# Optimization experiments

Hardware: AMD Instinct MI355X
Metric: run time of the kernel (lower is better)

The kernel has to match this reference:

```python
import jax, jax.numpy as jnp
import numpy as np

B, D, H, E, K = 8192, 1024, 4096, 8, 2
LOSS_COEF = 0.01
EPS_COMBINE = float(np.finfo(np.float64).eps)  # np.finfo(float).eps used in combine


def setup_inputs() -> dict:
    key = jax.random.key(0)
    ks = jax.random.split(key, 6)
    s_in = 1.0 / np.sqrt(D)
    s_hid = 1.0 / np.sqrt(H)
    return {
        "x": jax.random.normal(ks[0], (B, D), jnp.float32),
        "w_gate": jax.random.uniform(ks[1], (E, D), jnp.float32, -s_in, s_in),
        "fc1_w": jax.random.uniform(ks[2], (E, H, D), jnp.float32, -s_in, s_in),
        "fc1_b": jax.random.uniform(ks[3], (E, H), jnp.float32, -s_in, s_in),
        "fc2_w": jax.random.uniform(ks[4], (E, D, H), jnp.float32, -s_hid, s_hid),
        "fc2_b": jax.random.uniform(ks[5], (E, D), jnp.float32, -s_hid, s_hid),
    }


def _cv_squared(v):
    # torch .var() uses ddof=1
    return jnp.var(v, ddof=1) / (jnp.mean(v) ** 2 + 1e-10)


def _top_k_gating(x, w_gate):
    # clean logits (noisy_gating=False): [B, E]
    logits = x @ w_gate.T
    top_vals, top_idx = jax.lax.top_k(logits, K + 1)  # min(k+1, E)
    topk_vals = top_vals[:, :K]
    topk_idx = top_idx[:, :K]
    topk_gates = jax.nn.softmax(topk_vals, axis=1)
    gates = jnp.zeros((x.shape[0], E), x.dtype)
    gates = gates.at[jnp.arange(x.shape[0])[:, None], topk_idx].set(topk_gates)
    return gates


def _forward(x, w_gate, fc1_w, fc1_b, fc2_w, fc2_b):
    gates = _top_k_gating(x, w_gate)            # [B, E], sparse (k nonzeros/row)
    importance = gates.sum(axis=0)              # [E]
    load = (gates > 0).sum(axis=0).astype(jnp.float32)
    loss = (_cv_squared(importance) + _cv_squared(load)) * LOSS_COEF

    # Dense-equivalent expert compute: tokens with gate==0 contribute 0 to the
    # combine, identical math to SparseDispatcher's gather/scatter.
    h = jnp.einsum('bd,ehd->beh', x, fc1_w) + fc1_b            # [B, E, H]
    h = jax.nn.gelu(h, approximate=False)                      # torch exact gelu
    o = jnp.einsum('beh,edh->bed', h, fc2_w) + fc2_b           # [B, E, D]
    log_p = jax.nn.log_softmax(o, axis=-1)                     # LogSoftmax(dim=1)

    # combine: exp, weight by gates, scatter-add, eps-fill, log
    combined = jnp.einsum('be,bed->bd', gates, jnp.exp(log_p)) # [B, D]
    combined = jnp.where(combined == 0, EPS_COMBINE, combined)
    y = jnp.log(combined)
    return y, loss


def reference(x, w_gate, fc1_w, fc1_b, fc2_w, fc2_b):
    return _forward(x, w_gate, fc1_w, fc1_b, fc2_w, fc2_b)
```

## Files before the change

kernel.cpp:

```cpp
#include <hip/hip_runtime.h>
#include <cstdint>
#include <cmath>

#define BT 8192
#define DD 1024
#define HH 4096
#define EE 8

typedef __attribute__((ext_vector_type(8))) short short8;
typedef __attribute__((ext_vector_type(4))) float f32x4;
typedef unsigned short u16;
typedef unsigned int u32;

__device__ __forceinline__ u16 f2bf(float f) {
    u32 u = __float_as_uint(f);
    u += 0x7FFFu + ((u >> 16) & 1u);
    return (u16)(u >> 16);
}

__device__ __forceinline__ void gld_lds16(const void* g, void* l) {
    __builtin_amdgcn_global_load_lds((__attribute__((address_space(1))) void*)g,
                                     (__attribute__((address_space(3))) void*)l,
                                     16, 0, 0);
}

__global__ void cvt_kernel(const float* __restrict__ src, u16* __restrict__ dst, int n8) {
    int i = blockIdx.x * blockDim.x + threadIdx.x;
    if (i >= n8) return;
    size_t base = (size_t)i * 8;
    float4 a = *(const float4*)(src + base);
    float4 b = *(const float4*)(src + base + 4);
    uint4 o;
    o.x = (u32)f2bf(a.x) | ((u32)f2bf(a.y) << 16);
    o.y = (u32)f2bf(a.z) | ((u32)f2bf(a.w) << 16);
    o.z = (u32)f2bf(b.x) | ((u32)f2bf(b.y) << 16);
    o.w = (u32)f2bf(b.z) | ((u32)f2bf(b.w) << 16);
    *(uint4*)(dst + base) = o;
}

__global__ void gating_kernel(const float* __restrict__ x, const float* __restrict__ wg,
                              float* __restrict__ gate_arr, int* __restrict__ list,
                              int* __restrict__ info,
                              int* __restrict__ counts, float* __restrict__ importance) {
    int wave = (blockIdx.x * blockDim.x + threadIdx.x) >> 6;
    int lane = threadIdx.x & 63;
    if (wave >= BT) return;
    const float* xr = x + (size_t)wave * DD;
    double acc[EE];
#pragma unroll
    for (int e = 0; e < EE; ++e) acc[e] = 0.0;
    for (int i = lane; i < DD; i += 64) {
        double xv = (double)xr[i];
#pragma unroll
        for (int e = 0; e < EE; ++e)
            acc[e] += xv * (double)wg[e * DD + i];
    }
#pragma unroll
    for (int e = 0; e < EE; ++e) {
        double v = acc[e];
        for (int off = 32; off; off >>= 1) v += __shfl_down(v, off, 64);
        acc[e] = v;
    }
    if (lane == 0) {
        int i0 = 0; double v0 = acc[0];
        for (int e = 1; e < EE; ++e) if (acc[e] > v0) { v0 = acc[e]; i0 = e; }
        int i1 = -1; double v1 = -1e300;
        for (int e = 0; e < EE; ++e) { if (e == i0) continue; if (acc[e] > v1) { v1 = acc[e]; i1 = e; } }
        double e1 = exp(v1 - v0);
        double s = 1.0 + e1;
        float g0 = (float)(1.0 / s);
        float g1 = (float)(e1 / s);
        gate_arr[2 * wave]     = g0;
        gate_arr[2 * wave + 1] = g1;
        atomicAdd(&importance[i0], g0);
        atomicAdd(&importance[i1], g1);
        int p0 = atomicAdd(&counts[i0], 1);
        list[i0 * BT + p0] = wave;
        int p1 = atomicAdd(&counts[i1], 1);
        list[i1 * BT + p1] = wave;
        info[2 * wave]     = (i0 << 16) | p0;
        info[2 * wave + 1] = (i1 << 16) | p1;
    }
}

__global__ void loss_kernel(const int* __restrict__ counts, const float* __restrict__ importance,
                            int* __restrict__ offs, float* __restrict__ out_loss) {
    if (threadIdx.x == 0 && blockIdx.x == 0) {
        double mi = 0, ml = 0;
        int off = 0;
        for (int e = 0; e < EE; e++) {
            offs[e] = off; off += counts[e];
            mi += (double)importance[e]; ml += (double)counts[e];
        }
        mi /= EE; ml /= EE;
        double vi = 0, vl = 0;
        for (int e = 0; e < EE; e++) {
            double di = (double)importance[e] - mi; vi += di * di;
            double dl = (double)counts[e] - ml;     vl += dl * dl;
        }
        vi /= (EE - 1); vl /= (EE - 1);
        double cv_i = vi / (mi * mi + 1e-10);
        double cv_l = vl / (ml * ml + 1e-10);
        *out_loss = (float)((cv_i + cv_l) * 0.01);
    }
}

__global__ void gather_x_kernel(const float* __restrict__ x, const int* __restrict__ list,
                                const int* __restrict__ counts, const int* __restrict__ offs,
                                u16* __restrict__ xg) {
    int r = blockIdx.x;
    int e = 0;
#pragma unroll
    for (int i = 1; i < EE; ++i) if (r >= offs[i]) e = i;
    int m = r - offs[e];
    if (m >= counts[e]) return;
    int token = list[e * BT + m];
    const float* src = x + (size_t)token * DD;
    u16* dst = xg + (size_t)r * DD;
    int i = threadIdx.x * 4;
    float4 a = *(const float4*)(src + i);
    uint2 o;
    o.x = (u32)f2bf(a.x) | ((u32)f2bf(a.y) << 16);
    o.y = (u32)f2bf(a.z) | ((u32)f2bf(a.w) << 16);
    *(uint2*)(dst + i) = o;
}

template <int K, int NT, bool GELU, bool GATHER>
__global__ __launch_bounds__(256) void moe_gemm(const u16* __restrict__ Asrc,
                                                const u16* __restrict__ Bsrc,
                                                const float* __restrict__ bias,
                                                const int* __restrict__ list,
                                                const int* __restrict__ counts,
                                                const int* __restrict__ offs,
                                                u16* __restrict__ outB,
                                                float* __restrict__ outF) {
    const int e = blockIdx.z;
    const int cnt = counts[e];
    const int mbase = blockIdx.y * 128;
    if (mbase >= cnt) return;
    const int mmax = cnt - mbase;
    const int rowbase = offs[e] + mbase;
    const int nbase = blockIdx.x * 128;
    const int tid = threadIdx.x;
    const int lane = tid & 63;
    const int wv = tid >> 6;

    __shared__ u16 As[128 * 32];
    __shared__ u16 Bs[128 * 32];
    __shared__ int rows_lds[128];

    if constexpr (GATHER) {
        if (tid < 128) {
            int m = min(tid, mmax - 1);
            rows_lds[tid] = list[e * BT + mbase + m];
        }
        __syncthreads();
    }

    const int myrow = tid & 127;
    const int kch = tid >> 7;
    size_t arow;
    if constexpr (GATHER) arow = (size_t)rows_lds[myrow];
    else                  arow = (size_t)(rowbase + min(myrow, mmax - 1));
    const u16* aptr = Asrc + arow * (size_t)K + kch * 8;
    const u16* bptr = Bsrc + ((size_t)e * NT + nbase + myrow) * (size_t)K + kch * 8;

    f32x4 acc[4][4] = {};
    const int moff = (wv >> 1) * 64;
    const int noff = (wv & 1) * 64;
    const int kq = lane >> 4;
    const int rsub = lane & 15;

    for (int k0 = 0; k0 < K; k0 += 32) {
        gld_lds16(aptr + k0,      &As[tid * 8]);
        gld_lds16(aptr + k0 + 16, &As[(tid + 256) * 8]);
        gld_lds16(bptr + k0,      &Bs[tid * 8]);
        gld_lds16(bptr + k0 + 16, &Bs[(tid + 256) * 8]);
        __syncthreads();
        short8 af[4], bfr[4];
#pragma unroll
        for (int mi = 0; mi < 4; mi++)
            af[mi] = *(const short8*)&As[(kq * 128 + moff + mi * 16 + rsub) * 8];
#pragma unroll
        for (int ni = 0; ni < 4; ni++)
            bfr[ni] = *(const short8*)&Bs[(kq * 128 + noff + ni * 16 + rsub) * 8];
#pragma unroll
        for (int mi = 0; mi < 4; mi++)
#pragma unroll
            for (int ni = 0; ni < 4; ni++)
                acc[mi][ni] = __builtin_amdgcn_mfma_f32_16x16x32_bf16(af[mi], bfr[ni], acc[mi][ni], 0, 0, 0);
        __syncthreads();
    }

    const int rq = (lane >> 4) * 4;
    float bvals[4];
#pragma unroll
    for (int ni = 0; ni < 4; ni++)
        bvals[ni] = bias[(size_t)e * NT + nbase + noff + ni * 16 + rsub];
#pragma unroll
    for (int mi = 0; mi < 4; mi++) {
#pragma unroll
        for (int r = 0; r < 4; r++) {
            int m = moff + mi * 16 + rq + r;
            if (m < mmax) {
                size_t ro = (size_t)(rowbase + m);
#pragma unroll
                for (int ni = 0; ni < 4; ni++) {
                    int n = nbase + noff + ni * 16 + rsub;
                    float v = acc[mi][ni][r] + bvals[ni];
                    if constexpr (GELU) {
                        v = 0.5f * v * (1.0f + erff(v * 0.7071067811865476f));
                        outB[ro * NT + n] = f2bf(v);
                    } else {
                        outF[ro * NT + n] = v;
                    }
                }
            }
        }
    }
}

__global__ void combine_kernel(const float* __restrict__ o, const float* __restrict__ gates,
                               const int* __restrict__ info, const int* __restrict__ offs,
                               float* __restrict__ y) {
    const int b = blockIdx.x;
    const int tid = threadIdx.x;
    const int lane = tid & 63, wv = tid >> 6;
    const int inf0 = info[2 * b], inf1 = info[2 * b + 1];
    const int r0i = offs[inf0 >> 16] + (inf0 & 0xffff);
    const int r1i = offs[inf1 >> 16] + (inf1 & 0xffff);
    const float* r0 = o + (size_t)r0i * DD;
    const float* r1 = o + (size_t)r1i * DD;
    float v0[4], v1[4];
#pragma unroll
    for (int j = 0; j < 4; j++) { v0[j] = r0[tid + 256 * j]; v1[j] = r1[tid + 256 * j]; }
    float m0 = fmaxf(fmaxf(v0[0], v0[1]), fmaxf(v0[2], v0[3]));
    float m1 = fmaxf(fmaxf(v1[0], v1[1]), fmaxf(v1[2], v1[3]));
#pragma unroll
    for (int off = 32; off; off >>= 1) {
        m0 = fmaxf(m0, __shfl_xor(m0, off, 64));
        m1 = fmaxf(m1, __shfl_xor(m1, off, 64));
    }
    __shared__ float sred[2][4];
    if (lane == 0) { sred[0][wv] = m0; sred[1][wv] = m1; }
    __syncthreads();
    m0 = fmaxf(fmaxf(sred[0][0], sred[0][1]), fmaxf(sred[0][2], sred[0][3]));
    m1 = fmaxf(fmaxf(sred[1][0], sred[1][1]), fmaxf(sred[1][2], sred[1][3]));
    float p0[4], p1[4], s0 = 0.f, s1 = 0.f;
#pragma unroll
    for (int j = 0; j < 4; j++) {
        p0[j] = expf(v0[j] - m0); s0 += p0[j];
        p1[j] = expf(v1[j] - m1); s1 += p1[j];
    }
#pragma unroll
    for (int off = 32; off; off >>= 1) {
        s0 += __shfl_xor(s0, off, 64);
        s1 += __shfl_xor(s1, off, 64);
    }
    __shared__ float sred2[2][4];
    if (lane == 0) { sred2[0][wv] = s0; sred2[1][wv] = s1; }
    __syncthreads();
    s0 = sred2[0][0] + sred2[0][1] + sred2[0][2] + sred2[0][3];
    s1 = sred2[1][0] + sred2[1][1] + sred2[1][2] + sred2[1][3];
    const float c0 = gates[2 * b] / s0;
    const float c1 = gates[2 * b + 1] / s1;
#pragma unroll
    for (int j = 0; j < 4; j++) {
        float c = p0[j] * c0 + p1[j] * c1;
        if (c == 0.f) c = 2.2204460492503131e-16f;
        y[(size_t)b * DD + tid + 256 * j] = logf(c);
    }
}

extern "C" void kernel_launch(void* const* d_in, const int* in_sizes, int n_in,
                              void* d_out, int out_size, void* d_ws, size_t ws_size,
                              hipStream_t stream) {
    const float* x     = (const float*)d_in[0];
    const float* wgate = (const float*)d_in[1];
    const float* fc1w  = (const float*)d_in[2];
    const float* fc1b  = (const float*)d_in[3];
    const float* fc2w  = (const float*)d_in[4];
    const float* fc2b  = (const float*)d_in[5];
    float* out = (float*)d_out;

    char* ws = (char*)d_ws;
    const size_t MB = 1024 * 1024;
    const bool big = ws_size >= 289 * MB;
    u16* w1b = (u16*)(ws);
    float* o = (float*)(ws);
    u16* w2b = (u16*)(ws + 64 * MB);
    u16* xb  = (u16*)(ws + 128 * MB);
    u16* h   = (u16*)(ws + (big ? 128 : 144) * MB);
    u16* xg  = (u16*)(ws + 256 * MB);
    char* meta = ws + (big ? 288 : 272) * MB;
    int* counts       = (int*)meta;
    int* offs         = (int*)(meta + 32);
    float* importance = (float*)(meta + 64);
    float* gate_arr   = (float*)(meta + 128);
    int* info         = (int*)(meta + 128 + 65536);
    int* list         = (int*)(meta + 128 + 131072);

    hipMemsetAsync(meta, 0, 96, stream);
    cvt_kernel<<<(EE * HH * DD / 8 + 255) / 256, 256, 0, stream>>>(fc1w, w1b, EE * HH * DD / 8);
    cvt_kernel<<<(EE * DD * HH / 8 + 255) / 256, 256, 0, stream>>>(fc2w, w2b, EE * DD * HH / 8);
    gating_kernel<<<BT / 4, 256, 0, stream>>>(x, wgate, gate_arr, list, info, counts, importance);
    loss_kernel<<<1, 64, 0, stream>>>(counts, importance, offs, out + (size_t)BT * DD);

    if (big) {
        gather_x_kernel<<<2 * BT, 256, 0, stream>>>(x, list, counts, offs, xg);
        moe_gemm<DD, HH, true, false><<<dim3(HH / 128, BT / 128, EE), 256, 0, stream>>>(
            xg, w1b, fc1b, nullptr, counts, offs, h, nullptr);
    } else {
        cvt_kernel<<<(BT * DD / 8 + 255) / 256, 256, 0, stream>>>(x, xb, BT * DD / 8);
        moe_gemm<DD, HH, true, true><<<dim3(HH / 128, BT / 128, EE), 256, 0, stream>>>(
            xb, w1b, fc1b, list, counts, offs, h, nullptr);
    }
    moe_gemm<HH, DD, false, false><<<dim3(DD / 128, BT / 128, EE), 256, 0, stream>>>(
        h, w2b, fc2b, nullptr, counts, offs, nullptr, o);
    combine_kernel<<<BT, 256, 0, stream>>>(o, gate_arr, info, offs, out);
}
```

Before: 1.322 ms.

## Use persistent per-expert tile scheduling and always pre-gather tokens

Replaces the 3D grid, which launched a block for every possible M tile of every expert and let most of them exit early, with a 1D grid. Each block is assigned an expert via blockIdx mod 8 and strides over that expert's real (M,N) tiles, so no blocks are launched for empty tiles. It also drops the fallback that gathered rows inside the GEMM and always uses the separate gather kernel, assuming the workspace is large enough. The fixed slot count per expert can leave load imbalance when expert token counts are skewed, because each expert gets the same number of blocks.

```diff
diff --git a/kernel.cpp b/kernel.cpp
--- a/kernel.cpp
+++ b/kernel.cpp
@@ -125,94 +125,91 @@
     *(uint2*)(dst + i) = o;
 }
 
-template <int K, int NT, bool GELU, bool GATHER>
+template <int K, int NT, bool GELU>
 __global__ __launch_bounds__(256) void moe_gemm(const u16* __restrict__ Asrc,
                                                 const u16* __restrict__ Bsrc,
                                                 const float* __restrict__ bias,
-                                                const int* __restrict__ list,
                                                 const int* __restrict__ counts,
                                                 const int* __restrict__ offs,
                                                 u16* __restrict__ outB,
                                                 float* __restrict__ outF) {
-    const int e = blockIdx.z;
+    const int e = blockIdx.x & 7;
+    const int slot = blockIdx.x >> 3;
+    const int slots = gridDim.x >> 3;
     const int cnt = counts[e];
-    const int mbase = blockIdx.y * 128;
-    if (mbase >= cnt) return;
-    const int mmax = cnt - mbase;
-    const int rowbase = offs[e] + mbase;
-    const int nbase = blockIdx.x * 128;
+    const int mt = (cnt + 127) >> 7;
+    const int work = mt * (NT / 128);
+    const int ebase = offs[e];
+
     const int tid = threadIdx.x;
     const int lane = tid & 63;
     const int wv = tid >> 6;
-
-    __shared__ u16 As[128 * 32];
-    __shared__ u16 Bs[128 * 32];
-    __shared__ int rows_lds[128];
-
-    if constexpr (GATHER) {
-        if (tid < 128) {
-            int m = min(tid, mmax - 1);
-            rows_lds[tid] = list[e * BT + mbase + m];
-        }
-        __syncthreads();
-    }
-
     const int myrow = tid & 127;
     const int kch = tid >> 7;
-    size_t arow;
-    if constexpr (GATHER) arow = (size_t)rows_lds[myrow];
-    else                  arow = (size_t)(rowbase + min(myrow, mmax - 1));
-    const u16* aptr = Asrc + arow * (size_t)K + kch * 8;
-    const u16* bptr = Bsrc + ((size_t)e * NT + nbase + myrow) * (size_t)K + kch * 8;
-
-    f32x4 acc[4][4] = {};
     const int moff = (wv >> 1) * 64;
     const int noff = (wv & 1) * 64;
     const int kq = lane >> 4;
     const int rsub = lane & 15;
-
-    for (int k0 = 0; k0 < K; k0 += 32) {
-        gld_lds16(aptr + k0,      &As[tid * 8]);
-        gld_lds16(aptr + k0 + 16, &As[(tid + 256) * 8]);
-        gld_lds16(bptr + k0,      &Bs[tid * 8]);
-        gld_lds16(bptr + k0 + 16, &Bs[(tid + 256) * 8]);
-        __syncthreads();
-        short8 af[4], bfr[4];
-#pragma unroll
-        for (int mi = 0; mi < 4; mi++)
-            af[mi] = *(const short8*)&As[(kq * 128 + moff + mi * 16 + rsub) * 8];
+    const int rq = (lane >> 4) * 4;
+
+    __shared__ u16 As[128 * 32];
+    __shared__ u16 Bs[128 * 32];
+
+    for (int w = slot; w < work; w += slots) {
+        const int ntile = w / mt;
+        const int mtile = w - ntile * mt;
+        const int mbase = mtile * 128;
+        const int nbase = ntile * 128;
+        const int mmax = cnt - mbase;
+        const int rowbase = ebase + mbase;
+
+        const size_t arow = (size_t)(rowbase + min(myrow, mmax - 1));
+        const u16* aptr = Asrc + arow * (size_t)K + kch * 8;
+        const u16* bptr = Bsrc + ((size_t)e * NT + nbase + myrow) * (size_t)K + kch * 8;
+
+        f32x4 acc[4][4] = {};
+        for (int k0 = 0; k0 < K; k0 += 32) {
+            gld_lds16(aptr + k0,      &As[tid * 8]);
+            gld_lds16(aptr + k0 + 16, &As[(tid + 256) * 8]);
+            gld_lds16(bptr + k0,      &Bs[tid * 8]);
+            gld_lds16(bptr + k0 + 16, &Bs[(tid + 256) * 8]);
+            __syncthreads();
+            short8 af[4], bfr[4];
+#pragma unroll
+            for (int mi = 0; mi < 4; mi++)
+                af[mi] = *(const short8*)&As[(kq * 128 + moff + mi * 16 + rsub) * 8];
+#pragma unroll
+            for (int ni = 0; ni < 4; ni++)
+                bfr[ni] = *(const short8*)&Bs[(kq * 128 + noff + ni * 16 + rsub) * 8];
+#pragma unroll
+            for (int mi = 0; mi < 4; mi++)
+#pragma unroll
+                for (int ni = 0; ni < 4; ni++)
+                    acc[mi][ni] = __builtin_amdgcn_mfma_f32_16x16x32_bf16(af[mi], bfr[ni], acc[mi][ni], 0, 0, 0);
+            __syncthreads();
+        }
+
+        float bvals[4];
 #pragma unroll
         for (int ni = 0; ni < 4; ni++)
-            bfr[ni] = *(const short8*)&Bs[(kq * 128 + noff + ni * 16 + rsub) * 8];
-#pragma unroll
-        for (int mi = 0; mi < 4; mi++)
-#pragma unroll
-            for (int ni = 0; ni < 4; ni++)
-                acc[mi][ni] = __builtin_amdgcn_mfma_f32_16x16x32_bf16(af[mi], bfr[ni], acc[mi][ni], 0, 0, 0);
-        __syncthreads();
-    }
-
-    const int rq = (lane >> 4) * 4;
-    float bvals[4];
-#pragma unroll
-    for (int ni = 0; ni < 4; ni++)
-        bvals[ni] = bias[(size_t)e * NT + nbase + noff + ni * 16 + rsub];
-#pragma unroll
-    for (int mi = 0; mi < 4; mi++) {
-#pragma unroll
-        for (int r = 0; r < 4; r++) {
-            int m = moff + mi * 16 + rq + r;
-            if (m < mmax) {
-                size_t ro = (size_t)(rowbase + m);
-#pragma unroll
-                for (int ni = 0; ni < 4; ni++) {
-                    int n = nbase + noff + ni * 16 + rsub;
-                    float v = acc[mi][ni][r] + bvals[ni];
-                    if constexpr (GELU) {
-                        v = 0.5f * v * (1.0f + erff(v * 0.7071067811865476f));
-                        outB[ro * NT + n] = f2bf(v);
-                    } else {
-                        outF[ro * NT + n] = v;
+            bvals[ni] = bias[(size_t)e * NT + nbase + noff + ni * 16 + rsub];
+#pragma unroll
+        for (int mi = 0; mi < 4; mi++) {
+#pragma unroll
+            for (int r = 0; r < 4; r++) {
+                int m = moff + mi * 16 + rq + r;
+                if (m < mmax) {
+                    size_t ro = (size_t)(rowbase + m);
+#pragma unroll
+                    for (int ni = 0; ni < 4; ni++) {
+                        int n = nbase + noff + ni * 16 + rsub;
+                        float v = acc[mi][ni][r] + bvals[ni];
+                        if constexpr (GELU) {
+                            v = 0.5f * v * (1.0f + erff(v * 0.7071067811865476f));
+                            outB[ro * NT + n] = f2bf(v);
+                        } else {
+                            outF[ro * NT + n] = v;
+                        }
                     }
                 }
             }
@@ -285,14 +282,12 @@
 
     char* ws = (char*)d_ws;
     const size_t MB = 1024 * 1024;
-    const bool big = ws_size >= 289 * MB;
     u16* w1b = (u16*)(ws);
     float* o = (float*)(ws);
     u16* w2b = (u16*)(ws + 64 * MB);
-    u16* xb  = (u16*)(ws + 128 * MB);
-    u16* h   = (u16*)(ws + (big ? 128 : 144) * MB);
+    u16* h   = (u16*)(ws + 128 * MB);
     u16* xg  = (u16*)(ws + 256 * MB);
-    char* meta = ws + (big ? 288 : 272) * MB;
+    char* meta = ws + 288 * MB;
     int* counts       = (int*)meta;
     int* offs         = (int*)(meta + 32);
     float* importance = (float*)(meta + 64);
@@ -305,17 +300,11 @@
     cvt_kernel<<<(EE * DD * HH / 8 + 255) / 256, 256, 0, stream>>>(fc2w, w2b, EE * DD * HH / 8);
     gating_kernel<<<BT / 4, 256, 0, stream>>>(x, wgate, gate_arr, list, info, counts, importance);
     loss_kernel<<<1, 64, 0, stream>>>(counts, importance, offs, out + (size_t)BT * DD);
-
-    if (big) {
-        gather_x_kernel<<<2 * BT, 256, 0, stream>>>(x, list, counts, offs, xg);
-        moe_gemm<DD, HH, true, false><<<dim3(HH / 128, BT / 128, EE), 256, 0, stream>>>(
-            xg, w1b, fc1b, nullptr, counts, offs, h, nullptr);
-    } else {
-        cvt_kernel<<<(BT * DD / 8 + 255) / 256, 256, 0, stream>>>(x, xb, BT * DD / 8);
-        moe_gemm<DD, HH, true, true><<<dim3(HH / 128, BT / 128, EE), 256, 0, stream>>>(
-            xb, w1b, fc1b, list, counts, offs, h, nullptr);
-    }
-    moe_gemm<HH, DD, false, false><<<dim3(DD / 128, BT / 128, EE), 256, 0, stream>>>(
-        h, w2b, fc2b, nullptr, counts, offs, nullptr, o);
+    gather_x_kernel<<<2 * BT, 256, 0, stream>>>(x, list, counts, offs, xg);
+
+    moe_gemm<DD, HH, true><<<8 * 544, 256, 0, stream>>>(
+        xg, w1b, fc1b, counts, offs, h, nullptr);
+    moe_gemm<HH, DD, false><<<8 * 136, 256, 0, stream>>>(
+        h, w2b, fc2b, counts, offs, nullptr, o);
     combine_kernel<<<BT, 256, 0, stream>>>(o, gate_arr, info, offs, out);
 }
```

Result: slower. 1.409 ms (+6.5%).
